# Optimization experiments

Measured on AMD Instinct MI355X. Metric: run time of the kernel, lower is better.

## Reference

```python
import jax, jax.numpy as jnp
import numpy as np

N_NODES = 50000
N_EDGES = 400000
B = 2
NUM_STEP = 2
# SAGEConv layer dims (in, out): conv1..conv6
LAYER_DIMS = [(64, 128), (128, 64), (64, 32), (32, 32), (64, 64), (128, 64)]


def setup_inputs() -> dict:
    key = jax.random.key(0)
    ks = jax.random.split(key, 4 + 3 * len(LAYER_DIMS))
    inp = {
        "in_feat": jax.random.normal(ks[0], (B, N_NODES, 64), dtype=jnp.float32),
        "src": jax.random.randint(ks[1], (N_EDGES,), 0, N_NODES, dtype=jnp.int32),
        "dst": jax.random.randint(ks[2], (N_EDGES,), 0, N_NODES, dtype=jnp.int32),
    }
    for i, (fin, fout) in enumerate(LAYER_DIMS, start=1):
        scale = jnp.float32(1.0 / np.sqrt(fin))
        inp[f"w_self{i}"] = jax.random.normal(ks[3 * i], (fin, fout), dtype=jnp.float32) * scale
        inp[f"w_neigh{i}"] = jax.random.normal(ks[3 * i + 1], (fin, fout), dtype=jnp.float32) * scale
        inp[f"b{i}"] = jnp.zeros((fout,), dtype=jnp.float32)
    return inp


def reference(in_feat, src, dst,
              w_self1, w_neigh1, b1, w_self2, w_neigh2, b2,
              w_self3, w_neigh3, b3, w_self4, w_neigh4, b4,
              w_self5, w_neigh5, b5, w_self6, w_neigh6, b6):
    # in_feat: [B, N, F] -> internal [N, B, F] (matches torch transpose(0,1))
    h = jnp.transpose(in_feat, (1, 0, 2))
    # in-degree per dst node for mean aggregation (0-degree nodes -> agg 0)
    deg = jax.ops.segment_sum(jnp.ones(src.shape[0], jnp.float32), dst,
                              num_segments=N_NODES)
    deg = jnp.maximum(deg, 1.0)[:, None, None]  # [N,1,1]

    def sage(x, ws, wn, b):
        # DGL SAGEConv (mean): fc_self(h) + fc_neigh(mean_{u in N(v)} h_u) + b
        agg = jax.ops.segment_sum(x[src], dst, num_segments=N_NODES) / deg
        return x @ ws + agg @ wn + b

    for _ in range(NUM_STEP):
        h1 = jax.nn.relu(sage(h, w_self1, w_neigh1, b1))
        h2 = jax.nn.relu(sage(h1, w_self2, w_neigh2, b2))
        h3 = jax.nn.relu(sage(h2, w_self3, w_neigh3, b3))
        h4 = jnp.concatenate(
            [jax.nn.relu(sage(h3, w_self4, w_neigh4, b4)), h3], axis=2)
        h5 = jnp.concatenate(
            [jax.nn.relu(sage(h4, w_self5, w_neigh5, b5)), h4], axis=2)
        h = sage(h5, w_self6, w_neigh6, b6)
    return jnp.transpose(h, (1, 0, 2))
```

## Files before the change

kernel.cpp:

```cpp
#include <hip/hip_runtime.h>

#define NN 50000
#define NE 400000
#define BB 2
#define ROWS (NN * BB)

#define SCAN_CHUNK 1024
#define SCAN_NB ((NN + SCAN_CHUNK - 1) / SCAN_CHUNK)

__device__ inline void fma4(float4& a, float s, const float4& w) {
    a.x = fmaf(s, w.x, a.x); a.y = fmaf(s, w.y, a.y);
    a.z = fmaf(s, w.z, a.z); a.w = fmaf(s, w.w, a.w);
}
__device__ inline void add4(float4& a, const float4& v) {
    a.x += v.x; a.y += v.y; a.z += v.z; a.w += v.w;
}
__device__ inline unsigned bf2(float a, float b) {
    unsigned ua = __float_as_uint(a); ua = (ua + 0x7FFFu + ((ua >> 16) & 1u)) >> 16;
    unsigned ub = __float_as_uint(b); ub = (ub + 0x7FFFu + ((ub >> 16) & 1u)) >> 16;
    return ua | (ub << 16);
}
__device__ inline void bfadd(float4& lo, float4& hi, uint4 v) {
    lo.x += __uint_as_float(v.x << 16); lo.y += __uint_as_float(v.x & 0xFFFF0000u);
    lo.z += __uint_as_float(v.y << 16); lo.w += __uint_as_float(v.y & 0xFFFF0000u);
    hi.x += __uint_as_float(v.z << 16); hi.y += __uint_as_float(v.z & 0xFFFF0000u);
    hi.z += __uint_as_float(v.w << 16); hi.w += __uint_as_float(v.w & 0xFFFF0000u);
}


__global__ void k_hist(const int* __restrict__ dst, int* __restrict__ deg) {
    int e = blockIdx.x * 256 + threadIdx.x;
    if (e < NE) atomicAdd(&deg[dst[e]], 1);
}

__global__ __launch_bounds__(256) void k_scan1(const int* __restrict__ deg,
                                               int* __restrict__ bsum) {
    int b = blockIdx.x, t = threadIdx.x;
    int base = b * SCAN_CHUNK + t * 4;
    int s = 0;
#pragma unroll
    for (int i = 0; i < 4; i++) {
        int idx = base + i;
        if (idx < NN) s += deg[idx];
    }
    for (int d = 32; d; d >>= 1) s += __shfl_down(s, d);
    __shared__ int ws[4];
    if ((t & 63) == 0) ws[t >> 6] = s;
    __syncthreads();
    if (t == 0) bsum[b] = ws[0] + ws[1] + ws[2] + ws[3];
}

__global__ void k_scan2(const int* __restrict__ bsum, int* __restrict__ boff,
                        int* __restrict__ rowoff_last) {
    int lane = threadIdx.x;
    int v = (lane < SCAN_NB) ? bsum[lane] : 0;
    int incl = v;
    for (int d = 1; d < 64; d <<= 1) {
        int o = __shfl_up(incl, d);
        if (lane >= d) incl += o;
    }
    if (lane < SCAN_NB) boff[lane] = incl - v;
    if (lane == 63) rowoff_last[0] = incl;
}

__global__ __launch_bounds__(256) void k_scan3(const int* __restrict__ deg,
                                               const int* __restrict__ boff,
                                               int* __restrict__ rowoff,
                                               int* __restrict__ cursor,
                                               float* __restrict__ rdeg) {
    int b = blockIdx.x, t = threadIdx.x;
    int lane = t & 63, wv = t >> 6;
    int base = b * SCAN_CHUNK + t * 4;
    int dv[4];
    int ts = 0;
#pragma unroll
    for (int i = 0; i < 4; i++) {
        int idx = base + i;
        dv[i] = (idx < NN) ? deg[idx] : 0;
        ts += dv[i];
    }
    int incl = ts;
    for (int d = 1; d < 64; d <<= 1) {
        int o = __shfl_up(incl, d);
        if (lane >= d) incl += o;
    }
    __shared__ int wsum[4];
    if (lane == 63) wsum[wv] = incl;
    __syncthreads();
    int wexc = 0;
    for (int w = 0; w < wv; w++) wexc += wsum[w];
    int run = boff[b] + wexc + (incl - ts);
#pragma unroll
    for (int i = 0; i < 4; i++) {
        int idx = base + i;
        if (idx < NN) {
            rowoff[idx] = run;
            cursor[idx] = run;
            rdeg[idx] = 1.0f / fmaxf((float)dv[i], 1.0f);
            run += dv[i];
        }
    }
}

__global__ void k_fill(const int* __restrict__ src, const int* __restrict__ dst,
                       int* __restrict__ cursor, int* __restrict__ csr) {
    int e = blockIdx.x * 256 + threadIdx.x;
    if (e >= NE) return;
    int pos = atomicAdd(&cursor[dst[e]], 1);
    csr[pos] = src[e];
}


__global__ void k_pack(const float4* __restrict__ in, uint4* __restrict__ out) {
    int t = blockIdx.x * 256 + threadIdx.x;
    if (t >= ROWS * 8) return;
    int r = t >> 3, k = t & 7;
    int n = r >> 1, b = r & 1;
    float4 a = in[(b * NN + n) * 16 + k * 2];
    float4 c = in[(b * NN + n) * 16 + k * 2 + 1];
    uint4 o;
    o.x = bf2(a.x, a.y); o.y = bf2(a.z, a.w);
    o.z = bf2(c.x, c.y); o.w = bf2(c.z, c.w);
    out[t] = o;
}

__global__ void k_gather_bf(const uint4* __restrict__ x, const int* __restrict__ csr,
                            const int* __restrict__ rowoff, const float* __restrict__ rdeg,
                            float4* __restrict__ out, int w8s, int xp8, int xo8,
                            int op4, int oo4) {
    int t = blockIdx.x * 256 + threadIdx.x;
    int n = t >> w8s, tid = t & ((1 << w8s) - 1);
    if (n >= NN) return;
    int beg = rowoff[n], end = rowoff[n + 1];
    int a0 = xo8 + tid;
    int xp2 = 2 * xp8;
    float4 a0l = {0.f,0.f,0.f,0.f}, a0h = {0.f,0.f,0.f,0.f};
    float4 a1l = {0.f,0.f,0.f,0.f}, a1h = {0.f,0.f,0.f,0.f};
    int j = beg;
    for (; j + 2 <= end; j += 2) {
        int s0 = csr[j], s1 = csr[j+1];
        int b0 = s0 * xp2 + a0, b1 = s1 * xp2 + a0;
        uint4 p0 = x[b0], q0 = x[b0 + xp8];
        uint4 p1 = x[b1], q1 = x[b1 + xp8];
        bfadd(a0l, a0h, p0); bfadd(a1l, a1h, q0);
        bfadd(a0l, a0h, p1); bfadd(a1l, a1h, q1);
    }
    if (j < end) {
        int s = csr[j];
        int b = s * xp2 + a0;
        bfadd(a0l, a0h, x[b]); bfadd(a1l, a1h, x[b + xp8]);
    }
    float rd = rdeg[n];
    float4 o0l = {a0l.x*rd, a0l.y*rd, a0l.z*rd, a0l.w*rd};
    float4 o0h = {a0h.x*rd, a0h.y*rd, a0h.z*rd, a0h.w*rd};
    float4 o1l = {a1l.x*rd, a1l.y*rd, a1l.z*rd, a1l.w*rd};
    float4 o1h = {a1h.x*rd, a1h.y*rd, a1h.z*rd, a1h.w*rd};
    int r0 = (2*n) * op4 + oo4 + 2*tid;
    int r1 = (2*n + 1) * op4 + oo4 + 2*tid;
    out[r0] = o0l; out[r0 + 1] = o0h;
    out[r1] = o1l; out[r1 + 1] = o1h;
}

template<int FIN, int FOUT, int MODE, bool RELU, bool TRANS, int RPT, int NCQ, bool OBF, bool DUAL>
__global__ __launch_bounds__(256) void k_gemm(
    const float* __restrict__ x, const float* __restrict__ agg,
    const float* __restrict__ w0, const float* __restrict__ w1,
    const float* __restrict__ bias, float* __restrict__ out,
    int xns4, int xbs4, int xo4, int apitch4, int aoff4, int ostride4, int ooff4,
    uint2* __restrict__ bfo, int bfp2, int bfo2)
{
    constexpr int NQ = FOUT / 4;
    constexpr int TX = NQ / NCQ;
    constexpr int TY = 256 / TX;
    constexpr int TM = TY * RPT;
    constexpr int W4 = FIN * NQ;
    constexpr int NW = (MODE == 1) ? 2 : 1;

    __shared__ float4 wlds[NW * W4];

    int t = threadIdx.x;
    const float4* w0v = (const float4*)w0;
    for (int i = t; i < W4; i += 256) wlds[i] = w0v[i];
    if (MODE == 1) {
        const float4* w1v = (const float4*)w1;
        for (int i = t; i < W4; i += 256) wlds[W4 + i] = w1v[i];
    }
    __syncthreads();

    int tx = t % TX, ty = t / TX;
    int rbase = blockIdx.x * TM + ty * RPT;

    int xb[RPT], ab[RPT];
#pragma unroll
    for (int i = 0; i < RPT; i++) {
        int r = rbase + i;
        r = r < ROWS ? r : ROWS - 1;
        xb[i] = (r >> 1) * xns4 + (r & 1) * xbs4 + xo4;
        ab[i] = r * apitch4 + aoff4;
    }

    float4 acc[RPT][NCQ];
#pragma unroll
    for (int i = 0; i < RPT; i++)
#pragma unroll
        for (int j = 0; j < NCQ; j++) acc[i][j] = make_float4(0.f, 0.f, 0.f, 0.f);

    const float4* xv4 = (const float4*)x;
    const float4* av4 = (const float4*)agg;

    for (int k4 = 0; k4 < FIN / 4; k4++) {
        float4 wq[4][NCQ], nq[4][NCQ];
#pragma unroll
        for (int u = 0; u < 4; u++)
#pragma unroll
            for (int j = 0; j < NCQ; j++) {
                wq[u][j] = wlds[(k4 * 4 + u) * NQ + tx + j * TX];
                if (MODE == 1) nq[u][j] = wlds[W4 + (k4 * 4 + u) * NQ + tx + j * TX];
            }
#pragma unroll
        for (int i = 0; i < RPT; i++) {
            float4 xv = xv4[xb[i] + k4];
#pragma unroll
            for (int j = 0; j < NCQ; j++) {
                fma4(acc[i][j], xv.x, wq[0][j]); fma4(acc[i][j], xv.y, wq[1][j]);
                fma4(acc[i][j], xv.z, wq[2][j]); fma4(acc[i][j], xv.w, wq[3][j]);
            }
            if (MODE == 1) {
                float4 av = av4[ab[i] + k4];
#pragma unroll
                for (int j = 0; j < NCQ; j++) {
                    fma4(acc[i][j], av.x, nq[0][j]); fma4(acc[i][j], av.y, nq[1][j]);
                    fma4(acc[i][j], av.z, nq[2][j]); fma4(acc[i][j], av.w, nq[3][j]);
                }
            }
        }
    }

    float4 b4[NCQ];
#pragma unroll
    for (int j = 0; j < NCQ; j++) {
        b4[j] = make_float4(0.f, 0.f, 0.f, 0.f);
        if (MODE != 0) b4[j] = *(const float4*)&bias[(tx + j * TX) * 4];
    }

#pragma unroll
    for (int i = 0; i < RPT; i++) {
        int r = rbase + i;
        if (r >= ROWS) continue;
#pragma unroll
        for (int j = 0; j < NCQ; j++) {
            int q = tx + j * TX;
            float4 v = acc[i][j];
            if (MODE == 2) {
                float4 ag = av4[ab[i] + q];
                add4(v, ag);
            }
            if (MODE != 0) add4(v, b4[j]);
            if (RELU) {
                v.x = fmaxf(v.x, 0.f); v.y = fmaxf(v.y, 0.f);
                v.z = fmaxf(v.z, 0.f); v.w = fmaxf(v.w, 0.f);
            }
            if (OBF) {
                uint2 w; w.x = bf2(v.x, v.y); w.y = bf2(v.z, v.w);
                ((uint2*)out)[r * ostride4 + ooff4 + q] = w;
            } else {
                int oidx;
                if (TRANS) {
                    int n = r >> 1, b = r & 1;
                    oidx = b * (NN * 16) + n * 16 + q;
                } else {
                    oidx = r * ostride4 + ooff4 + q;
                }
                ((float4*)out)[oidx] = v;
            }
            if (DUAL) {
                uint2 w; w.x = bf2(v.x, v.y); w.y = bf2(v.z, v.w);
                bfo[r * bfp2 + bfo2 + q] = w;
            }
        }
    }
}


template<int FIN, int FOUT, int MODE, bool RELU, bool TRANS,
         int RPT = 8, int NCQ = 1, bool OBF = false, bool DUAL = false>
static void launch_gemm(const float* x, const float* agg, const float* w0, const float* w1,
                        const float* bias, float* out, int xns4, int xbs4, int xo4,
                        int apitch4, int aoff4, int ostride4, int ooff4,
                        hipStream_t stream,
                        uint2* bfo = nullptr, int bfp2 = 0, int bfo2 = 0) {
    constexpr int TM = (256 / (FOUT / 4 / NCQ)) * RPT;
    int nb = (ROWS + TM - 1) / TM;
    k_gemm<FIN, FOUT, MODE, RELU, TRANS, RPT, NCQ, OBF, DUAL><<<nb, 256, 0, stream>>>(
        x, agg, w0, w1, bias, out, xns4, xbs4, xo4, apitch4, aoff4, ostride4, ooff4,
        bfo, bfp2, bfo2);
}

static void launch_gather_bf(const void* xbf, const int* csr, const int* rowoff,
                             const float* rdeg, float* aggb, int width,
                             int xp8, int xo8, int op4, int oo4, hipStream_t stream) {
    int w8s = 0;
    while ((1 << w8s) < width / 8) w8s++;
    int gt = NN << w8s;
    k_gather_bf<<<(gt + 255) / 256, 256, 0, stream>>>(
        (const uint4*)xbf, csr, rowoff, rdeg, (float4*)aggb, w8s, xp8, xo8, op4, oo4);
}

extern "C" void kernel_launch(void* const* d_in, const int* in_sizes, int n_in,
                              void* d_out, int out_size, void* d_ws, size_t ws_size,
                              hipStream_t stream) {
    const float* in_feat = (const float*)d_in[0];
    const int* src = (const int*)d_in[1];
    const int* dst = (const int*)d_in[2];
    const float* Ws[6], *Wn[6], *Bi[6];
    for (int i = 0; i < 6; i++) {
        Ws[i] = (const float*)d_in[3 + 3 * i];
        Wn[i] = (const float*)d_in[4 + 3 * i];
        Bi[i] = (const float*)d_in[5 + 3 * i];
    }

    char* ws = (char*)d_ws;
    size_t off = 0;
    auto alloc = [&](size_t bytes) {
        void* p = ws + off;
        off = (off + bytes + 255) & ~(size_t)255;
        return p;
    };
    float* rdeg   = (float*)alloc((size_t)NN * 4);
    int*   deg    = (int*)  alloc((size_t)NN * 4);
    int*   rowoff = (int*)  alloc((size_t)(NN + 1) * 4);
    int*   cursor = (int*)  alloc((size_t)NN * 4);
    int*   csr    = (int*)  alloc((size_t)NE * 4);
    int*   bsum   = (int*)  alloc((size_t)SCAN_NB * 4);
    int*   boff   = (int*)  alloc((size_t)SCAN_NB * 4);
    float* bufH   = (float*)alloc((size_t)ROWS * 64 * 4);
    float* bufA   = (float*)alloc((size_t)ROWS * 128 * 4);
    float* bufB   = (float*)alloc((size_t)ROWS * 128 * 4);
    float* aggb   = (float*)alloc((size_t)ROWS * 64 * 4);
    float* zbuf   = (float*)d_out;

    uint2* hbf  = (uint2*)bufA;
    uint2* b3bf = (uint2*)(bufA + (size_t)ROWS * 32);

    hipMemsetAsync(deg, 0, (size_t)NN * 4, stream);
    k_hist<<<(NE + 255) / 256, 256, 0, stream>>>(dst, deg);
    k_scan1<<<SCAN_NB, 256, 0, stream>>>(deg, bsum);
    k_scan2<<<1, 64, 0, stream>>>(bsum, boff, rowoff + NN);
    k_scan3<<<SCAN_NB, 256, 0, stream>>>(deg, boff, rowoff, cursor, rdeg);
    k_fill<<<(NE + 255) / 256, 256, 0, stream>>>(src, dst, cursor, csr);

    k_pack<<<(ROWS * 8 + 255) / 256, 256, 0, stream>>>((const float4*)in_feat, (uint4*)hbf);

    const int BSTR = NN * 16;

    for (int s = 0; s < 2; s++) {
        int last = (s == 1);
        const float* hx = s ? bufH : in_feat;
        int hns = s ? 32 : 16, hbs = s ? 16 : BSTR;

        launch_gather_bf(hbf, csr, rowoff, rdeg, aggb, 64, 8, 0, 16, 0, stream);
        launch_gemm<64, 128, 1, true, false, 8, 2>(hx, aggb, Ws[0], Wn[0], Bi[0],
                                                   bufA, hns, hbs, 0, 16, 0, 32, 0, stream);

        launch_gemm<128, 64, 0, false, false, 8, 2, true>(
            bufA, nullptr, Wn[1], nullptr, nullptr, zbuf, 64, 32, 0, 0, 0, 16, 0, stream);
        launch_gather_bf(zbuf, csr, rowoff, rdeg, aggb, 64, 8, 0, 16, 0, stream);
        launch_gemm<128, 64, 2, true, false, 8, 2>(bufA, aggb, Ws[1], nullptr, Bi[1],
                                                   bufH, 64, 32, 0, 16, 0, 16, 0, stream);

        launch_gemm<64, 32, 0, false, false, 8, 1, true>(
            bufH, nullptr, Wn[2], nullptr, nullptr, zbuf, 32, 16, 0, 0, 0, 8, 0, stream);
        launch_gather_bf(zbuf, csr, rowoff, rdeg, aggb, 32, 4, 0, 8, 0, stream);
        launch_gemm<64, 32, 2, true, false, 8, 1, false, true>(
            bufH, aggb, Ws[2], nullptr, Bi[2], bufB, 32, 16, 0, 8, 0, 32, 24, stream,
            b3bf, 16, 8);

        launch_gather_bf(b3bf, csr, rowoff, rdeg, aggb, 32, 8, 4, 16, 8, stream);
        launch_gemm<32, 32, 1, true, false, 8, 1, false, true>(
            bufB, aggb, Ws[3], Wn[3], Bi[3], bufB, 64, 32, 24, 16, 8, 32, 16, stream,
            b3bf, 16, 0);

        launch_gather_bf(b3bf, csr, rowoff, rdeg, aggb, 32, 8, 0, 16, 0, stream);
        launch_gemm<64, 64, 1, true, false, 8, 2>(bufB, aggb, Ws[4], Wn[4], Bi[4],
                                                  bufB, 64, 32, 16, 16, 0, 32, 0, stream);

        launch_gemm<128, 64, 0, false, false, 8, 2, true>(
            bufB, nullptr, Wn[5], nullptr, nullptr, zbuf, 64, 32, 0, 0, 0, 16, 0, stream);
        launch_gather_bf(zbuf, csr, rowoff, rdeg, aggb, 64, 8, 0, 16, 0, stream);
        if (last) {
            launch_gemm<128, 64, 2, false, true, 8, 2>(bufB, aggb, Ws[5], nullptr, Bi[5],
                                                       (float*)d_out, 64, 32, 0, 16, 0, 16, 0, stream);
        } else {
            launch_gemm<128, 64, 2, false, false, 8, 2, false, true>(
                bufB, aggb, Ws[5], nullptr, Bi[5], bufH, 64, 32, 0, 16, 0, 16, 0, stream,
                hbf, 16, 0);
        }
    }
}
```

Before: 977.1 us.

## Use bf16 MFMA for neighbor projections and split layer-1 GEMM

Adds a bf16 MFMA kernel that computes the pre-aggregation neighbor projections for layers 2 and 6 (x @ Wn) straight from bf16 copies of the activations. The producing GEMMs now also write those bf16 copies. Layer 1 is split: the aggregated input is projected first into a bf16 temporary, and the self-term GEMM then adds it in. The aim is to move the largest FLOP-heavy projections onto matrix cores and cut fp32 traffic. The cost is one extra GEMM launch in layer 1 and more bf16 rounding in intermediate values.

```diff
diff --git a/kernel.cpp b/kernel.cpp
--- a/kernel.cpp
+++ b/kernel.cpp
@@ -8,6 +8,9 @@
 #define SCAN_CHUNK 1024
 #define SCAN_NB ((NN + SCAN_CHUNK - 1) / SCAN_CHUNK)
 
+typedef float f32x4 __attribute__((ext_vector_type(4)));
+typedef short s16x8 __attribute__((ext_vector_type(8)));
+
 __device__ inline void fma4(float4& a, float s, const float4& w) {
     a.x = fmaf(s, w.x, a.x); a.y = fmaf(s, w.y, a.y);
     a.z = fmaf(s, w.z, a.z); a.w = fmaf(s, w.w, a.w);
@@ -15,10 +18,12 @@
 __device__ inline void add4(float4& a, const float4& v) {
     a.x += v.x; a.y += v.y; a.z += v.z; a.w += v.w;
 }
+__device__ inline unsigned bf1(float v) {
+    unsigned u = __float_as_uint(v);
+    return (u + 0x7FFFu + ((u >> 16) & 1u)) >> 16;
+}
 __device__ inline unsigned bf2(float a, float b) {
-    unsigned ua = __float_as_uint(a); ua = (ua + 0x7FFFu + ((ua >> 16) & 1u)) >> 16;
-    unsigned ub = __float_as_uint(b); ub = (ub + 0x7FFFu + ((ub >> 16) & 1u)) >> 16;
-    return ua | (ub << 16);
+    return bf1(a) | (bf1(b) << 16);
 }
 __device__ inline void bfadd(float4& lo, float4& hi, uint4 v) {
     lo.x += __uint_as_float(v.x << 16); lo.y += __uint_as_float(v.x & 0xFFFF0000u);
@@ -161,7 +166,58 @@
     out[r1] = o1l; out[r1 + 1] = o1h;
 }
 
-template<int FIN, int FOUT, int MODE, bool RELU, bool TRANS, int RPT, int NCQ, bool OBF, bool DUAL>
+__global__ __launch_bounds__(256) void k_zmfma(
+    const uint4* __restrict__ a0, int p0, const uint4* __restrict__ a1, int p1,
+    const float* __restrict__ w, unsigned short* __restrict__ z)
+{
+    __shared__ float wl[128 * 64];
+    int t = threadIdx.x;
+    for (int i = t; i < 2048; i += 256)
+        ((float4*)wl)[i] = ((const float4*)w)[i];
+    __syncthreads();
+
+    int lane = t & 63, wv = t >> 6;
+    int row16 = lane & 15, kq = lane >> 4;
+
+    s16x8 bf[4][4];
+#pragma unroll
+    for (int kt = 0; kt < 4; kt++)
+#pragma unroll
+        for (int nt = 0; nt < 4; nt++) {
+            s16x8 b;
+#pragma unroll
+            for (int j = 0; j < 8; j++)
+                b[j] = (short)bf1(wl[(kt*32 + kq*8 + j)*64 + nt*16 + row16]);
+            bf[kt][nt] = b;
+        }
+
+    for (int mt = blockIdx.x * 4 + wv; mt < ROWS / 16; mt += gridDim.x * 4) {
+        int r = mt * 16 + row16;
+        s16x8 av[4];
+        av[0] = __builtin_bit_cast(s16x8, a0[r * p0 + kq]);
+        av[1] = __builtin_bit_cast(s16x8, a0[r * p0 + 4 + kq]);
+        av[2] = __builtin_bit_cast(s16x8, a1[r * p1 + kq]);
+        av[3] = __builtin_bit_cast(s16x8, a1[r * p1 + 4 + kq]);
+        f32x4 acc[4] = {{0.f,0.f,0.f,0.f},{0.f,0.f,0.f,0.f},
+                        {0.f,0.f,0.f,0.f},{0.f,0.f,0.f,0.f}};
+#pragma unroll
+        for (int kt = 0; kt < 4; kt++)
+#pragma unroll
+            for (int nt = 0; nt < 4; nt++)
+                acc[nt] = __builtin_amdgcn_mfma_f32_16x16x32_bf16(
+                    av[kt], bf[kt][nt], acc[nt], 0, 0, 0);
+#pragma unroll
+        for (int nt = 0; nt < 4; nt++)
+#pragma unroll
+            for (int i = 0; i < 4; i++) {
+                int ro = mt * 16 + kq * 4 + i;
+                z[ro * 64 + nt * 16 + row16] = (unsigned short)bf1(acc[nt][i]);
+            }
+    }
+}
+
+template<int FIN, int FOUT, int MODE, bool RELU, bool TRANS,
+         int RPT, int NCQ, bool OBF, bool DUAL, bool ABF>
 __global__ __launch_bounds__(256) void k_gemm(
     const float* __restrict__ x, const float* __restrict__ agg,
     const float* __restrict__ w0, const float* __restrict__ w1,
@@ -252,8 +308,16 @@
             int q = tx + j * TX;
             float4 v = acc[i][j];
             if (MODE == 2) {
-                float4 ag = av4[ab[i] + q];
-                add4(v, ag);
+                if (ABF) {
+                    uint2 u = ((const uint2*)agg)[ab[i] + q];
+                    v.x += __uint_as_float(u.x << 16);
+                    v.y += __uint_as_float(u.x & 0xFFFF0000u);
+                    v.z += __uint_as_float(u.y << 16);
+                    v.w += __uint_as_float(u.y & 0xFFFF0000u);
+                } else {
+                    float4 ag = av4[ab[i] + q];
+                    add4(v, ag);
+                }
             }
             if (MODE != 0) add4(v, b4[j]);
             if (RELU) {
@@ -283,7 +347,7 @@
 
 
 template<int FIN, int FOUT, int MODE, bool RELU, bool TRANS,
-         int RPT = 8, int NCQ = 1, bool OBF = false, bool DUAL = false>
+         int RPT = 8, int NCQ = 1, bool OBF = false, bool DUAL = false, bool ABF = false>
 static void launch_gemm(const float* x, const float* agg, const float* w0, const float* w1,
                         const float* bias, float* out, int xns4, int xbs4, int xo4,
                         int apitch4, int aoff4, int ostride4, int ooff4,
@@ -291,7 +355,7 @@
                         uint2* bfo = nullptr, int bfp2 = 0, int bfo2 = 0) {
     constexpr int TM = (256 / (FOUT / 4 / NCQ)) * RPT;
     int nb = (ROWS + TM - 1) / TM;
-    k_gemm<FIN, FOUT, MODE, RELU, TRANS, RPT, NCQ, OBF, DUAL><<<nb, 256, 0, stream>>>(
+    k_gemm<FIN, FOUT, MODE, RELU, TRANS, RPT, NCQ, OBF, DUAL, ABF><<<nb, 256, 0, stream>>>(
         x, agg, w0, w1, bias, out, xns4, xbs4, xo4, apitch4, aoff4, ostride4, ooff4,
         bfo, bfp2, bfo2);
 }
@@ -341,6 +405,9 @@
 
     uint2* hbf  = (uint2*)bufA;
     uint2* b3bf = (uint2*)(bufA + (size_t)ROWS * 32);
+    uint2* c5bf = (uint2*)(bufA + (size_t)ROWS * 64);
+    uint2* tmp1 = (uint2*)bufB;
+    uint2* h1bf = (uint2*)(bufB + (size_t)ROWS * 64);
 
     hipMemsetAsync(deg, 0, (size_t)NN * 4, stream);
     k_hist<<<(NE + 255) / 256, 256, 0, stream>>>(dst, deg);
@@ -359,11 +426,16 @@
         int hns = s ? 32 : 16, hbs = s ? 16 : BSTR;
 
         launch_gather_bf(hbf, csr, rowoff, rdeg, aggb, 64, 8, 0, 16, 0, stream);
-        launch_gemm<64, 128, 1, true, false, 8, 2>(hx, aggb, Ws[0], Wn[0], Bi[0],
-                                                   bufA, hns, hbs, 0, 16, 0, 32, 0, stream);
-
-        launch_gemm<128, 64, 0, false, false, 8, 2, true>(
-            bufA, nullptr, Wn[1], nullptr, nullptr, zbuf, 64, 32, 0, 0, 0, 16, 0, stream);
+        launch_gemm<64, 128, 0, false, false, 8, 2, true>(
+            aggb, nullptr, Wn[0], nullptr, nullptr, (float*)tmp1,
+            32, 16, 0, 0, 0, 32, 0, stream);
+        launch_gemm<64, 128, 2, true, false, 8, 2, false, true, true>(
+            hx, (const float*)tmp1, Ws[0], nullptr, Bi[0], bufA,
+            hns, hbs, 0, 32, 0, 32, 0, stream, h1bf, 32, 0);
+
+        k_zmfma<<<256, 256, 0, stream>>>(
+            (const uint4*)h1bf, 16, (const uint4*)h1bf + 8, 16, Wn[1],
+            (unsigned short*)zbuf);
         launch_gather_bf(zbuf, csr, rowoff, rdeg, aggb, 64, 8, 0, 16, 0, stream);
         launch_gemm<128, 64, 2, true, false, 8, 2>(bufA, aggb, Ws[1], nullptr, Bi[1],
                                                    bufH, 64, 32, 0, 16, 0, 16, 0, stream);
@@ -381,11 +453,13 @@
             b3bf, 16, 0);
 
         launch_gather_bf(b3bf, csr, rowoff, rdeg, aggb, 32, 8, 0, 16, 0, stream);
-        launch_gemm<64, 64, 1, true, false, 8, 2>(bufB, aggb, Ws[4], Wn[4], Bi[4],
-                                                  bufB, 64, 32, 16, 16, 0, 32, 0, stream);
-
-        launch_gemm<128, 64, 0, false, false, 8, 2, true>(
-            bufB, nullptr, Wn[5], nullptr, nullptr, zbuf, 64, 32, 0, 0, 0, 16, 0, stream);
+        launch_gemm<64, 64, 1, true, false, 8, 2, false, true>(
+            bufB, aggb, Ws[4], Wn[4], Bi[4], bufB, 64, 32, 16, 16, 0, 32, 0, stream,
+            c5bf, 16, 0);
+
+        k_zmfma<<<256, 256, 0, stream>>>(
+            (const uint4*)c5bf, 8, (const uint4*)b3bf, 8, Wn[5],
+            (unsigned short*)zbuf);
         launch_gather_bf(zbuf, csr, rowoff, rdeg, aggb, 64, 8, 0, 16, 0, stream);
         if (last) {
             launch_gemm<128, 64, 2, false, true, 8, 2>(bufB, aggb, Ws[5], nullptr, Bi[5],
```

New measurement: 914.4 us. 1.07x faster.
